# Kernel optimization log

Measured on AMD Instinct MI355X. Metric: run time of the kernel, lower is better.

Reference implementation:

```python
import jax, jax.numpy as jnp
import numpy as np

D_MODEL = 1024
N_HEADS = 16
D_HEAD = D_MODEL // N_HEADS
M_SLOPE = 0.5
BATCH = 2
SEQ = 2048


def setup_inputs() -> dict:
    key = jax.random.key(0)
    k1, k2, k3 = jax.random.split(key, 3)
    x = jax.random.normal(k1, (BATCH, SEQ, D_MODEL), dtype=jnp.float32)
    qkv_w = jax.random.normal(k2, (3 * D_MODEL, D_MODEL), dtype=jnp.float32) * (1.0 / np.sqrt(D_MODEL))
    qkv_b = jnp.zeros((3 * D_MODEL,), dtype=jnp.float32)
    out_w = jax.random.normal(k3, (D_MODEL, D_MODEL), dtype=jnp.float32) * (1.0 / np.sqrt(D_MODEL))
    out_b = jnp.zeros((D_MODEL,), dtype=jnp.float32)
    return {"x": x, "qkv_w": qkv_w, "qkv_b": qkv_b, "out_w": out_w, "out_b": out_b}


def _alibi_bias(n_heads, seq_len, m, dtype):
    # bias[h, i, j] = -|i - j| * m**h
    slopes = (m ** jnp.arange(n_heads, dtype=dtype))  # (H,)
    pos = jnp.arange(seq_len, dtype=dtype)
    dist = jnp.abs(pos[:, None] - pos[None, :])  # (S, S)
    return -dist[None, :, :] * slopes[:, None, None]  # (H, S, S)


def reference(x, qkv_w, qkv_b, out_w, out_b):
    batch, seq_len, d_model = x.shape
    qkv = x @ qkv_w.T + qkv_b  # (B, S, 3*D)
    qkv = qkv.reshape(batch, seq_len, N_HEADS, 3 * D_HEAD).transpose(0, 2, 1, 3)  # (B, H, S, 3*dh)
    q, k, v = jnp.split(qkv, 3, axis=-1)  # each (B, H, S, dh)
    scale = jnp.sqrt(jnp.asarray(D_HEAD, dtype=x.dtype))
    scores = jnp.einsum('bhid,bhjd->bhij', q, k) / scale  # (B, H, S, S)
    scores = scores + _alibi_bias(N_HEADS, seq_len, M_SLOPE, x.dtype)[None]
    attn = jax.nn.softmax(scores, axis=-1)
    out = jnp.einsum('bhij,bhjd->bhid', attn, v)  # (B, H, S, dh)
    out = out.transpose(0, 2, 1, 3).reshape(batch, seq_len, d_model)
    return out @ out_w.T + out_b
```

## Files before the change

kernel.cpp:

```cpp
#include <hip/hip_runtime.h>
#include <hip/hip_bf16.h>
#include <cstdint>
#include <cstddef>

typedef _Float16 half8 __attribute__((ext_vector_type(8)));
typedef _Float16 half4 __attribute__((ext_vector_type(4)));
typedef float floatx4 __attribute__((ext_vector_type(4)));

#define LOG2E 1.4426950408889634f

__device__ __forceinline__ void async_load16(const void* g, void* l) {
  void* gnc = const_cast<void*>(g);
  __builtin_amdgcn_global_load_lds(
      (__attribute__((address_space(1))) void*)(gnc),
      (__attribute__((address_space(3))) void*)(l), 16, 0, 0);
}

__global__ __launch_bounds__(256) void cvt_all(const float* __restrict__ x,
                                               const float* __restrict__ w1,
                                               const float* __restrict__ w2,
                                               _Float16* __restrict__ xh,
                                               _Float16* __restrict__ w1h,
                                               _Float16* __restrict__ w2h) {
  int i = blockIdx.x * 256 + threadIdx.x;
  const float* src;
  _Float16* dst;
  int off;
  if (i < 1048576) {
    src = x; dst = xh; off = i;
  } else if (i < 1048576 + 786432) {
    src = w1; dst = w1h; off = i - 1048576;
  } else {
    src = w2; dst = w2h; off = i - 1835008;
  }
  float4 v = reinterpret_cast<const float4*>(src)[off];
  half4 h = {(_Float16)v.x, (_Float16)v.y, (_Float16)v.z, (_Float16)v.w};
  reinterpret_cast<half4*>(dst)[off] = h;
}

__global__ __launch_bounds__(256) void qkv_gemm(const _Float16* __restrict__ X,
                                                const _Float16* __restrict__ W,
                                                const float* __restrict__ bias,
                                                _Float16* __restrict__ Q,
                                                _Float16* __restrict__ K,
                                                _Float16* __restrict__ V) {
  __shared__ _Float16 As[128 * 32];
  __shared__ _Float16 Bs[128 * 32];
  const int tid = threadIdx.x;
  const int lane = tid & 63, wid = tid >> 6;
  const int lr = lane & 15, lg = lane >> 4;
  const int bm = blockIdx.x, bn = blockIdx.y;
  const int wm = wid >> 1, wn = wid & 1;
  floatx4 acc[4][4] = {};

  for (int kt = 0; kt < 32; ++kt) {
    const int k0 = kt * 32;
    __syncthreads();
#pragma unroll
    for (int it = 0; it < 2; ++it) {
      int c = it * 256 + (wid << 6) + lane;
      int r = c >> 2, slot = c & 3;
      int cc = slot ^ ((r >> 1) & 3);
      async_load16(X + (size_t)(bm * 128 + r) * 1024 + k0 + cc * 8,
                   &As[(it * 256 + (wid << 6)) * 8]);
      async_load16(W + (size_t)(bn * 128 + r) * 1024 + k0 + cc * 8,
                   &Bs[(it * 256 + (wid << 6)) * 8]);
    }
    __syncthreads();
    half8 a[4], b[4];
#pragma unroll
    for (int mi = 0; mi < 4; ++mi) {
      int row = wm * 64 + mi * 16 + lr;
      int slot = lg ^ ((row >> 1) & 3);
      a[mi] = *(const half8*)&As[row * 32 + slot * 8];
    }
#pragma unroll
    for (int nj = 0; nj < 4; ++nj) {
      int row = wn * 64 + nj * 16 + lr;
      int slot = lg ^ ((row >> 1) & 3);
      b[nj] = *(const half8*)&Bs[row * 32 + slot * 8];
    }
#pragma unroll
    for (int mi = 0; mi < 4; ++mi)
#pragma unroll
      for (int nj = 0; nj < 4; ++nj)
        acc[mi][nj] = __builtin_amdgcn_mfma_f32_16x16x32_f16(a[mi], b[nj], acc[mi][nj], 0, 0, 0);
  }

#pragma unroll
  for (int nj = 0; nj < 4; ++nj) {
    int j = bn * 128 + wn * 64 + nj * 16 + lr;
    float bj = bias[j];
    int h = j / 192, rr = j % 192;
    int typ = rr >> 6, d = rr & 63;
    _Float16* dst = (typ == 0) ? Q : (typ == 1) ? K : V;
#pragma unroll
    for (int mi = 0; mi < 4; ++mi) {
#pragma unroll
      for (int r = 0; r < 4; ++r) {
        int i = bm * 128 + wm * 64 + mi * 16 + lg * 4 + r;
        int b_ = i >> 11, s = i & 2047;
        float v = acc[mi][nj][r] + bj;
        dst[(size_t)((b_ * 16 + h) * 2048 + s) * 64 + d] = (_Float16)v;
      }
    }
  }
}

__global__ __launch_bounds__(256) void transpose_v(const _Float16* __restrict__ V,
                                                   _Float16* __restrict__ Vt) {
  __shared__ _Float16 tile[64 * 80];
  const int t = threadIdx.x;
  const int s0 = blockIdx.x * 64;
  const int bh = blockIdx.y;
  const _Float16* src = V + (size_t)bh * 131072;
#pragma unroll
  for (int it = 0; it < 2; ++it) {
    int c = it * 256 + t;
    int rs = c >> 3, ch = c & 7;
    half8 v = *(const half8*)(src + (size_t)(s0 + rs) * 64 + ch * 8);
    *(half8*)&tile[rs * 80 + ch * 8] = v;
  }
  __syncthreads();
  _Float16* dst = Vt + (size_t)bh * 131072;
  int rd = t >> 2, cs = t & 3;
#pragma unroll
  for (int hf = 0; hf < 2; ++hf) {
    half8 v;
#pragma unroll
    for (int k = 0; k < 8; ++k) {
      int s = cs * 16 + hf * 8 + k;
      v[k] = tile[s * 80 + rd];
    }
    *(half8*)(dst + (size_t)rd * 2048 + s0 + cs * 16 + hf * 8) = v;
  }
}

__global__ __launch_bounds__(256, 4) void attn(const _Float16* __restrict__ Q,
                                               const _Float16* __restrict__ K,
                                               const _Float16* __restrict__ Vt,
                                               _Float16* __restrict__ O) {
  __shared__ _Float16 KPs[128 * 64];
  __shared__ _Float16 Vs[64 * 128];
  const int tid = threadIdx.x, lane = tid & 63, wid = tid >> 6;
  const int lr = lane & 15, lg = lane >> 4;
  const int qt = blockIdx.x, bh = blockIdx.y;
  const int h = bh & 15, b = bh >> 4;
  const int q0 = qt * 64 + wid * 16;
  const float slopeL2 = exp2f(-(float)h) * LOG2E;
  const float qscale = 0.125f * LOG2E;
  const float Mfix = 8.0f;
  const _Float16* Qg = Q + (size_t)bh * 131072;
  const _Float16* Kg = K + (size_t)bh * 131072;
  const _Float16* Vg = Vt + (size_t)bh * 131072;

  half8 qa[2];
#pragma unroll
  for (int kf = 0; kf < 2; ++kf)
    qa[kf] = *(const half8*)(Qg + (size_t)(q0 + lr) * 64 + kf * 32 + lg * 8);

  float lsum[4] = {0.f, 0.f, 0.f, 0.f};
  floatx4 o[4] = {};
  _Float16* Pw = &KPs[wid * 2048];
  const int ibase = q0 + lg * 4 - lr;

  for (int kt = 0; kt < 16; ++kt) {
    const int kv0 = kt * 128;
    __syncthreads();
#pragma unroll
    for (int it = 0; it < 4; ++it) {
      int c = it * 256 + (wid << 6) + lane;
      {
        int r = c >> 3, slot = c & 7, cc = slot ^ (r & 7);
        async_load16(Kg + (size_t)(kv0 + r) * 64 + cc * 8, &KPs[(it * 256 + (wid << 6)) * 8]);
      }
      {
        int r = c >> 4, slot = c & 15, cc = slot ^ (r & 15);
        async_load16(Vg + (size_t)r * 2048 + kv0 + cc * 8, &Vs[(it * 256 + (wid << 6)) * 8]);
      }
    }
    __syncthreads();

    floatx4 sc[8];
#pragma unroll
    for (int nj = 0; nj < 8; ++nj) sc[nj] = floatx4{0.f, 0.f, 0.f, 0.f};
#pragma unroll
    for (int nj = 0; nj < 8; ++nj) {
      int row = nj * 16 + lr;
#pragma unroll
      for (int kf = 0; kf < 2; ++kf) {
        int slot = (kf * 4 + lg) ^ (row & 7);
        half8 kb = *(const half8*)&KPs[row * 64 + slot * 8];
        sc[nj] = __builtin_amdgcn_mfma_f32_16x16x32_f16(qa[kf], kb, sc[nj], 0, 0, 0);
      }
    }
    __syncthreads();

#pragma unroll
    for (int r = 0; r < 4; ++r) {
      int prow = lg * 4 + r;
      float fj = (float)(ibase + r - kv0);
#pragma unroll
      for (int nj = 0; nj < 8; ++nj) {
        float t = fmaf(sc[nj][r], qscale, fmaf(fabsf(fj), -slopeL2, -Mfix));
        float p = __builtin_amdgcn_exp2f(t);
        lsum[r] += p;
        int col = nj * 16 + lr;
        int slot = (col >> 3) ^ (prow & 7);
        Pw[prow * 128 + slot * 8 + (col & 7)] = (_Float16)p;
        fj -= 16.0f;
      }
    }

#pragma unroll
    for (int kf2 = 0; kf2 < 4; ++kf2) {
      int slotp = (kf2 * 4 + lg) ^ (lr & 7);
      half8 pa = *(const half8*)&Pw[lr * 128 + slotp * 8];
#pragma unroll
      for (int nd = 0; nd < 4; ++nd) {
        int vrow = nd * 16 + lr;
        int slotv = (kf2 * 4 + lg) ^ (vrow & 15);
        half8 vb = *(const half8*)&Vs[vrow * 128 + slotv * 8];
        o[nd] = __builtin_amdgcn_mfma_f32_16x16x32_f16(pa, vb, o[nd], 0, 0, 0);
      }
    }
  }

#pragma unroll
  for (int r = 0; r < 4; ++r) {
#pragma unroll
    for (int x = 1; x < 16; x <<= 1) lsum[r] += __shfl_xor(lsum[r], x, 64);
  }
#pragma unroll
  for (int r = 0; r < 4; ++r) {
    float inv = 1.0f / lsum[r];
    int s = q0 + lg * 4 + r;
#pragma unroll
    for (int nd = 0; nd < 4; ++nd) {
      int d = nd * 16 + lr;
      O[((size_t)(b * 2048 + s)) * 1024 + h * 64 + d] = (_Float16)(o[nd][r] * inv);
    }
  }
}

__global__ __launch_bounds__(256) void out_gemm(const _Float16* __restrict__ A_,
                                                const _Float16* __restrict__ W,
                                                const float* __restrict__ bias,
                                                float* __restrict__ out) {
  __shared__ _Float16 As[128 * 32];
  __shared__ _Float16 Bs[128 * 32];
  const int tid = threadIdx.x;
  const int lane = tid & 63, wid = tid >> 6;
  const int lr = lane & 15, lg = lane >> 4;
  const int bm = blockIdx.x, bn = blockIdx.y;
  const int wm = wid >> 1, wn = wid & 1;
  floatx4 acc[4][4] = {};

  for (int kt = 0; kt < 32; ++kt) {
    const int k0 = kt * 32;
    __syncthreads();
#pragma unroll
    for (int it = 0; it < 2; ++it) {
      int c = it * 256 + (wid << 6) + lane;
      int r = c >> 2, slot = c & 3;
      int cc = slot ^ ((r >> 1) & 3);
      async_load16(A_ + (size_t)(bm * 128 + r) * 1024 + k0 + cc * 8,
                   &As[(it * 256 + (wid << 6)) * 8]);
      async_load16(W + (size_t)(bn * 128 + r) * 1024 + k0 + cc * 8,
                   &Bs[(it * 256 + (wid << 6)) * 8]);
    }
    __syncthreads();
    half8 a[4], b[4];
#pragma unroll
    for (int mi = 0; mi < 4; ++mi) {
      int row = wm * 64 + mi * 16 + lr;
      int slot = lg ^ ((row >> 1) & 3);
      a[mi] = *(const half8*)&As[row * 32 + slot * 8];
    }
#pragma unroll
    for (int nj = 0; nj < 4; ++nj) {
      int row = wn * 64 + nj * 16 + lr;
      int slot = lg ^ ((row >> 1) & 3);
      b[nj] = *(const half8*)&Bs[row * 32 + slot * 8];
    }
#pragma unroll
    for (int mi = 0; mi < 4; ++mi)
#pragma unroll
      for (int nj = 0; nj < 4; ++nj)
        acc[mi][nj] = __builtin_amdgcn_mfma_f32_16x16x32_f16(a[mi], b[nj], acc[mi][nj], 0, 0, 0);
  }

#pragma unroll
  for (int nj = 0; nj < 4; ++nj) {
    int j = bn * 128 + wn * 64 + nj * 16 + lr;
    float bj = bias[j];
#pragma unroll
    for (int mi = 0; mi < 4; ++mi) {
#pragma unroll
      for (int r = 0; r < 4; ++r) {
        int i = bm * 128 + wm * 64 + mi * 16 + lg * 4 + r;
        out[(size_t)i * 1024 + j] = acc[mi][nj][r] + bj;
      }
    }
  }
}

extern "C" void kernel_launch(void* const* d_in, const int* in_sizes, int n_in,
                              void* d_out, int out_size, void* d_ws, size_t ws_size,
                              hipStream_t stream) {
  const float* x = (const float*)d_in[0];
  const float* qkv_w = (const float*)d_in[1];
  const float* qkv_b = (const float*)d_in[2];
  const float* out_w = (const float*)d_in[3];
  const float* out_b = (const float*)d_in[4];
  float* out = (float*)d_out;
  char* ws = (char*)d_ws;

  _Float16* xh = (_Float16*)(ws + 0);
  _Float16* wqh = (_Float16*)(ws + 8388608);
  _Float16* woh = (_Float16*)(ws + 14680064);
  _Float16* Qh = (_Float16*)(ws + 16777216);
  _Float16* Kh = (_Float16*)(ws + 25165824);
  _Float16* Vh = (_Float16*)(ws + 33554432);
  _Float16* Vth = (_Float16*)(ws + 41943040);
  _Float16* Oh = (_Float16*)(ws + 50331648);

  cvt_all<<<8192, 256, 0, stream>>>(x, qkv_w, out_w, xh, wqh, woh);
  qkv_gemm<<<dim3(32, 24), 256, 0, stream>>>(xh, wqh, qkv_b, Qh, Kh, Vh);
  transpose_v<<<dim3(32, 32), 256, 0, stream>>>(Vh, Vth);
  attn<<<dim3(32, 32), 256, 0, stream>>>(Qh, Kh, Vth, Oh);
  out_gemm<<<dim3(32, 8), 256, 0, stream>>>(Oh, woh, out_b, out);
}
```

Baseline: 206.3 us.

## Double-buffer attention KV tiles, fold Q scale into GEMM, permute V layout

The attention kernel now uses 64-key tiles with double-buffered async LDS loads, so the next K/V tile is fetched while the current one is computed, and one barrier per iteration replaces three. The Q softmax scale is folded into the QKV GEMM epilogue, and the fixed max offset is dropped. V is transposed into a permuted key order so each lane's P values can be written as one packed half4 store using cvt_pkrtz. MFMA sections are wrapped in s_setprio. Risks include fp16 overflow or accuracy loss from removing the -8 offset and from rounding the pre-scaled Q to fp16.

```diff
diff --git a/kernel.cpp b/kernel.cpp
--- a/kernel.cpp
+++ b/kernel.cpp
@@ -5,15 +5,21 @@
 
 typedef _Float16 half8 __attribute__((ext_vector_type(8)));
 typedef _Float16 half4 __attribute__((ext_vector_type(4)));
+typedef _Float16 half2v __attribute__((ext_vector_type(2)));
 typedef float floatx4 __attribute__((ext_vector_type(4)));
 
 #define LOG2E 1.4426950408889634f
+#define QSCALE (0.125f * LOG2E)
 
 __device__ __forceinline__ void async_load16(const void* g, void* l) {
   void* gnc = const_cast<void*>(g);
   __builtin_amdgcn_global_load_lds(
       (__attribute__((address_space(1))) void*)(gnc),
       (__attribute__((address_space(3))) void*)(l), 16, 0, 0);
+}
+
+__device__ __forceinline__ half2v cvt_pk_f16(float a, float b) {
+  return __builtin_bit_cast(half2v, __builtin_amdgcn_cvt_pkrtz(a, b));
 }
 
 __global__ __launch_bounds__(256) void cvt_all(const float* __restrict__ x,
@@ -93,6 +99,7 @@
     float bj = bias[j];
     int h = j / 192, rr = j % 192;
     int typ = rr >> 6, d = rr & 63;
+    float scl = (typ == 0) ? QSCALE : 1.0f;
     _Float16* dst = (typ == 0) ? Q : (typ == 1) ? K : V;
 #pragma unroll
     for (int mi = 0; mi < 4; ++mi) {
@@ -100,7 +107,7 @@
       for (int r = 0; r < 4; ++r) {
         int i = bm * 128 + wm * 64 + mi * 16 + lg * 4 + r;
         int b_ = i >> 11, s = i & 2047;
-        float v = acc[mi][nj][r] + bj;
+        float v = (acc[mi][nj][r] + bj) * scl;
         dst[(size_t)((b_ * 16 + h) * 2048 + s) * 64 + d] = (_Float16)v;
       }
     }
@@ -108,51 +115,50 @@
 }
 
 __global__ __launch_bounds__(256) void transpose_v(const _Float16* __restrict__ V,
-                                                   _Float16* __restrict__ Vt) {
-  __shared__ _Float16 tile[64 * 80];
+                                                   _Float16* __restrict__ Vp) {
+  __shared__ _Float16 tile[128 * 72];
   const int t = threadIdx.x;
-  const int s0 = blockIdx.x * 64;
+  const int s0 = blockIdx.x * 128;
   const int bh = blockIdx.y;
   const _Float16* src = V + (size_t)bh * 131072;
 #pragma unroll
-  for (int it = 0; it < 2; ++it) {
+  for (int it = 0; it < 4; ++it) {
     int c = it * 256 + t;
     int rs = c >> 3, ch = c & 7;
     half8 v = *(const half8*)(src + (size_t)(s0 + rs) * 64 + ch * 8);
-    *(half8*)&tile[rs * 80 + ch * 8] = v;
+    *(half8*)&tile[rs * 72 + ch * 8] = v;
   }
   __syncthreads();
-  _Float16* dst = Vt + (size_t)bh * 131072;
-  int rd = t >> 2, cs = t & 3;
-#pragma unroll
-  for (int hf = 0; hf < 2; ++hf) {
+  _Float16* dst = Vp + (size_t)bh * 131072;
+  const int rd = t >> 2, q4 = t & 3;
+#pragma unroll
+  for (int qq = 0; qq < 4; ++qq) {
     half8 v;
 #pragma unroll
-    for (int k = 0; k < 8; ++k) {
-      int s = cs * 16 + hf * 8 + k;
-      v[k] = tile[s * 80 + rd];
-    }
-    *(half8*)(dst + (size_t)rd * 2048 + s0 + cs * 16 + hf * 8) = v;
+    for (int e = 0; e < 8; ++e) {
+      int p = q4 * 32 + qq * 8 + e;
+      int blk = p >> 6, u = p & 63;
+      int key = (u & 3) * 16 + (u >> 2);
+      v[e] = tile[(blk * 64 + key) * 72 + rd];
+    }
+    *(half8*)(dst + (size_t)rd * 2048 + s0 + q4 * 32 + qq * 8) = v;
   }
 }
 
 __global__ __launch_bounds__(256, 4) void attn(const _Float16* __restrict__ Q,
                                                const _Float16* __restrict__ K,
-                                               const _Float16* __restrict__ Vt,
+                                               const _Float16* __restrict__ Vp,
                                                _Float16* __restrict__ O) {
-  __shared__ _Float16 KPs[128 * 64];
-  __shared__ _Float16 Vs[64 * 128];
+  __shared__ _Float16 lds[20480];
   const int tid = threadIdx.x, lane = tid & 63, wid = tid >> 6;
   const int lr = lane & 15, lg = lane >> 4;
   const int qt = blockIdx.x, bh = blockIdx.y;
   const int h = bh & 15, b = bh >> 4;
   const int q0 = qt * 64 + wid * 16;
   const float slopeL2 = exp2f(-(float)h) * LOG2E;
-  const float qscale = 0.125f * LOG2E;
-  const float Mfix = 8.0f;
   const _Float16* Qg = Q + (size_t)bh * 131072;
   const _Float16* Kg = K + (size_t)bh * 131072;
-  const _Float16* Vg = Vt + (size_t)bh * 131072;
+  const _Float16* Vg = Vp + (size_t)bh * 131072;
 
   half8 qa[2];
 #pragma unroll
@@ -161,69 +167,81 @@
 
   float lsum[4] = {0.f, 0.f, 0.f, 0.f};
   floatx4 o[4] = {};
-  _Float16* Pw = &KPs[wid * 2048];
-  const int ibase = q0 + lg * 4 - lr;
-
-  for (int kt = 0; kt < 16; ++kt) {
-    const int kv0 = kt * 128;
-    __syncthreads();
-#pragma unroll
-    for (int it = 0; it < 4; ++it) {
+  _Float16* Pw = &lds[16384 + wid * 1024];
+
+  auto stage = [&](int kt, int bsel) {
+    const int kv0 = kt * 64;
+#pragma unroll
+    for (int it = 0; it < 2; ++it) {
       int c = it * 256 + (wid << 6) + lane;
-      {
-        int r = c >> 3, slot = c & 7, cc = slot ^ (r & 7);
-        async_load16(Kg + (size_t)(kv0 + r) * 64 + cc * 8, &KPs[(it * 256 + (wid << 6)) * 8]);
-      }
-      {
-        int r = c >> 4, slot = c & 15, cc = slot ^ (r & 15);
-        async_load16(Vg + (size_t)r * 2048 + kv0 + cc * 8, &Vs[(it * 256 + (wid << 6)) * 8]);
-      }
-    }
-    __syncthreads();
-
-    floatx4 sc[8];
-#pragma unroll
-    for (int nj = 0; nj < 8; ++nj) sc[nj] = floatx4{0.f, 0.f, 0.f, 0.f};
-#pragma unroll
-    for (int nj = 0; nj < 8; ++nj) {
+      int rk = c >> 3, sk = c & 7, ck = sk ^ (rk & 7);
+      async_load16(Kg + (size_t)(kv0 + rk) * 64 + ck * 8,
+                   &lds[bsel * 4096 + (it * 256 + (wid << 6)) * 8]);
+      async_load16(Vg + (size_t)rk * 2048 + kv0 + ck * 8,
+                   &lds[8192 + bsel * 4096 + (it * 256 + (wid << 6)) * 8]);
+    }
+  };
+
+  stage(0, 0);
+  __syncthreads();
+
+  for (int kt = 0; kt < 32; ++kt) {
+    const int cur = kt & 1;
+    const int kv0 = kt * 64;
+    if (kt < 31) stage(kt + 1, cur ^ 1);
+    const _Float16* Kb = &lds[cur * 4096];
+    const _Float16* Vb = &lds[8192 + cur * 4096];
+
+    floatx4 sc[4];
+#pragma unroll
+    for (int nj = 0; nj < 4; ++nj) sc[nj] = floatx4{0.f, 0.f, 0.f, 0.f};
+    __builtin_amdgcn_s_setprio(1);
+#pragma unroll
+    for (int nj = 0; nj < 4; ++nj) {
       int row = nj * 16 + lr;
 #pragma unroll
       for (int kf = 0; kf < 2; ++kf) {
         int slot = (kf * 4 + lg) ^ (row & 7);
-        half8 kb = *(const half8*)&KPs[row * 64 + slot * 8];
+        half8 kb = *(const half8*)&Kb[row * 64 + slot * 8];
         sc[nj] = __builtin_amdgcn_mfma_f32_16x16x32_f16(qa[kf], kb, sc[nj], 0, 0, 0);
       }
     }
-    __syncthreads();
-
+    __builtin_amdgcn_s_setprio(0);
+
+    const int ibase = q0 + lg * 4 - lr - kv0;
 #pragma unroll
     for (int r = 0; r < 4; ++r) {
-      int prow = lg * 4 + r;
-      float fj = (float)(ibase + r - kv0);
-#pragma unroll
-      for (int nj = 0; nj < 8; ++nj) {
-        float t = fmaf(sc[nj][r], qscale, fmaf(fabsf(fj), -slopeL2, -Mfix));
-        float p = __builtin_amdgcn_exp2f(t);
-        lsum[r] += p;
-        int col = nj * 16 + lr;
-        int slot = (col >> 3) ^ (prow & 7);
-        Pw[prow * 128 + slot * 8 + (col & 7)] = (_Float16)p;
+      const int prow = lg * 4 + r;
+      float fj = (float)(ibase + r);
+      float p[4];
+#pragma unroll
+      for (int nj = 0; nj < 4; ++nj) {
+        float t = fmaf(fabsf(fj), -slopeL2, sc[nj][r]);
+        p[nj] = __builtin_amdgcn_exp2f(t);
         fj -= 16.0f;
       }
-    }
-
-#pragma unroll
-    for (int kf2 = 0; kf2 < 4; ++kf2) {
-      int slotp = (kf2 * 4 + lg) ^ (lr & 7);
-      half8 pa = *(const half8*)&Pw[lr * 128 + slotp * 8];
+      lsum[r] += (p[0] + p[1]) + (p[2] + p[3]);
+      union { half4 h4; half2v h2[2]; } u;
+      u.h2[0] = cvt_pk_f16(p[0], p[1]);
+      u.h2[1] = cvt_pk_f16(p[2], p[3]);
+      *(half4*)&Pw[prow * 64 + (lr ^ ((prow & 7) << 1)) * 4] = u.h4;
+    }
+
+    __builtin_amdgcn_s_setprio(1);
+#pragma unroll
+    for (int kf2 = 0; kf2 < 2; ++kf2) {
+      int slotp = ((kf2 << 2) + lg) ^ (lr & 7);
+      half8 pa = *(const half8*)&Pw[lr * 64 + slotp * 8];
 #pragma unroll
       for (int nd = 0; nd < 4; ++nd) {
         int vrow = nd * 16 + lr;
-        int slotv = (kf2 * 4 + lg) ^ (vrow & 15);
-        half8 vb = *(const half8*)&Vs[vrow * 128 + slotv * 8];
+        int slotv = ((kf2 << 2) + lg) ^ (vrow & 7);
+        half8 vb = *(const half8*)&Vb[vrow * 64 + slotv * 8];
         o[nd] = __builtin_amdgcn_mfma_f32_16x16x32_f16(pa, vb, o[nd], 0, 0, 0);
       }
     }
+    __builtin_amdgcn_s_setprio(0);
+    if (kt < 31) __syncthreads();
   }
 
 #pragma unroll
@@ -322,12 +340,12 @@
   _Float16* Qh = (_Float16*)(ws + 16777216);
   _Float16* Kh = (_Float16*)(ws + 25165824);
   _Float16* Vh = (_Float16*)(ws + 33554432);
-  _Float16* Vth = (_Float16*)(ws + 41943040);
+  _Float16* Vph = (_Float16*)(ws + 41943040);
   _Float16* Oh = (_Float16*)(ws + 50331648);
 
   cvt_all<<<8192, 256, 0, stream>>>(x, qkv_w, out_w, xh, wqh, woh);
   qkv_gemm<<<dim3(32, 24), 256, 0, stream>>>(xh, wqh, qkv_b, Qh, Kh, Vh);
-  transpose_v<<<dim3(32, 32), 256, 0, stream>>>(Vh, Vth);
-  attn<<<dim3(32, 32), 256, 0, stream>>>(Qh, Kh, Vth, Oh);
+  transpose_v<<<dim3(16, 32), 256, 0, stream>>>(Vh, Vph);
+  attn<<<dim3(32, 32), 256, 0, stream>>>(Qh, Kh, Vph, Oh);
   out_gemm<<<dim3(32, 8), 256, 0, stream>>>(Oh, woh, out_b, out);
 }
```

Result: faster. 198.2 us (-3.9%).
